# Optimization experiments

Measured on AMD Instinct MI355X. Metric: run time of the kernel, lower is better.

Reference implementation:

```python
import jax, jax.numpy as jnp
import numpy as np

D_MODEL = 512
NUM_HEADS = 8
D_HEAD = 64
B, T = 8, 1024


def sinusoidal_pos(start, end, d, dtype=jnp.float32):
    # positions start .. end-1, standard sinusoidal encoding, shape (1, end-start, d)
    pos = jnp.arange(start, end, dtype=jnp.float32)[:, None]              # (L,1)
    inv_freq = jnp.exp(-jnp.log(10000.0) * jnp.arange(0, d, 2, dtype=jnp.float32) / d)
    ang = pos * inv_freq[None, :]                                          # (L,d/2)
    pe = jnp.stack([jnp.sin(ang), jnp.cos(ang)], axis=-1).reshape(pos.shape[0], d)
    return pe[None].astype(dtype)                                          # (1,L,d)


def _relative_shift(x):
    # x: (B,H,T,L) -> Transformer-XL shift trick
    b, h, t, l = x.shape
    x = jnp.pad(x, ((0, 0), (0, 0), (0, 0), (1, 0)))                       # (B,H,T,L+1)
    x = x.reshape(b, h, l + 1, t)[:, :, 1:, :].reshape(b, h, t, l)
    return x


def setup_inputs() -> dict:
    key = jax.random.key(0)
    ks = jax.random.split(key, 8)
    hd = NUM_HEADS * D_HEAD
    s_in = 1.0 / np.sqrt(D_MODEL)
    s_out = 1.0 / np.sqrt(hd)
    return {
        "xs": jax.random.normal(ks[0], (B, T, D_MODEL), jnp.float32),
        "mask": jnp.ones((B, T, T), jnp.int32),
        "Wq": jax.random.normal(ks[1], (D_MODEL, hd), jnp.float32) * s_in,
        "Wk": jax.random.normal(ks[2], (D_MODEL, hd), jnp.float32) * s_in,
        "Wv": jax.random.normal(ks[3], (D_MODEL, hd), jnp.float32) * s_in,
        "Wpos": jax.random.normal(ks[4], (D_MODEL, hd), jnp.float32) * s_in,
        "Wout": jax.random.normal(ks[5], (hd, D_MODEL), jnp.float32) * s_out,
        "u_bias": jax.random.normal(ks[6], (NUM_HEADS, D_HEAD), jnp.float32) * 0.02,
        "v_bias": jax.random.normal(ks[7], (NUM_HEADS, D_HEAD), jnp.float32) * 0.02,
    }


def reference(xs, mask, Wq, Wk, Wv, Wpos, Wout, u_bias, v_bias):
    b, t, _ = xs.shape
    scale = 1.0 / np.sqrt(D_HEAD)

    def split_heads(y):  # (B,T,H*dh) -> (B,H,T,dh)
        return y.reshape(b, t, NUM_HEADS, D_HEAD).transpose(0, 2, 1, 3)

    q = split_heads(xs @ Wq)
    k = split_heads(xs @ Wk)
    v = split_heads(xs @ Wv)

    # positions -(T-1) .. T-1, length 2T-1
    pos_enc = sinusoidal_pos(-(t - 1), t, D_MODEL, xs.dtype)               # (1,L,D)
    p = (pos_enc[0] @ Wpos).reshape(-1, NUM_HEADS, D_HEAD).transpose(1, 0, 2)  # (H,L,dh)

    q_u = q + u_bias[None, :, None, :]
    q_v = q + v_bias[None, :, None, :]

    matrix_ac = jnp.einsum("bhtd,bhsd->bhts", q_u, k)                      # (B,H,T,T)
    matrix_bd = jnp.einsum("bhtd,hld->bhtl", q_v, p)                       # (B,H,T,2T-1)
    matrix_bd = _relative_shift(matrix_bd)[:, :, :, :t]                    # (B,H,T,T)

    scores = (matrix_ac + matrix_bd) * scale

    m = (mask[:, None, :, :] == 0)                                          # (B,1,T,T)
    scores = jnp.where(m, -jnp.inf, scores)
    attn = jax.nn.softmax(scores, axis=-1)
    attn = jnp.where(m, 0.0, attn)
    # dropout is identity in eval mode

    z = jnp.einsum("bhts,bhsd->bthd", attn, v).reshape(b, t, NUM_HEADS * D_HEAD)
    return z @ Wout
```

## Files before the change

kernel.cpp:

```cpp
#include <hip/hip_runtime.h>
#include <hip/hip_bf16.h>


typedef unsigned short u16;
typedef unsigned long long u64;
typedef unsigned int u32;
typedef __attribute__((ext_vector_type(8))) short bf16x8;
typedef __attribute__((ext_vector_type(8))) unsigned short ushort8v;
typedef __attribute__((ext_vector_type(4))) float floatx4;

__device__ __forceinline__ float b2f(u16 u) {
    union { unsigned int i; float f; } x; x.i = ((unsigned int)u) << 16; return x.f;
}
__device__ __forceinline__ u16 f2b(float f) {
    __hip_bfloat16 h = __float2bfloat16(f);
    return *reinterpret_cast<u16*>(&h);
}

#define MFMA16(a, b, c) __builtin_amdgcn_mfma_f32_16x16x32_bf16(a, b, c, 0, 0, 0)

__device__ __forceinline__ void gll16(const u16* g, u16* l) {
    __builtin_amdgcn_global_load_lds(
        (const __attribute__((address_space(1))) u32*)g,
        (__attribute__((address_space(3))) u32*)l, 16, 0, 0);
}

__global__ __launch_bounds__(256) void prep_kernel(
    const float* __restrict__ X, u16* __restrict__ Xb,
    const float* __restrict__ W0, const float* __restrict__ W1,
    const float* __restrict__ W2, const float* __restrict__ W3,
    const float* __restrict__ W4, u16* __restrict__ WT,
    const int* __restrict__ mask, u64* __restrict__ Mp,
    u16* __restrict__ Peb)
{
    const int bi = blockIdx.x;
    const int tid = threadIdx.x;
    if (bi < 2048) {
        size_t i = ((size_t)bi * 256 + tid) * 8;
        float4 a = *(const float4*)&X[i];
        float4 b = *(const float4*)&X[i + 4];
        ushort8v s;
        s[0] = f2b(a.x); s[1] = f2b(a.y); s[2] = f2b(a.z); s[3] = f2b(a.w);
        s[4] = f2b(b.x); s[5] = f2b(b.y); s[6] = f2b(b.z); s[7] = f2b(b.w);
        *(ushort8v*)&Xb[i] = s;
    } else if (bi < 2368) {
        __shared__ float t[64][68];
        const int li = bi - 2048;
        const int m = li >> 6;
        const float* src = (m == 0) ? W0 : (m == 1) ? W1 : (m == 2) ? W2
                         : (m == 3) ? W3 : W4;
        u16* dst = WT + (size_t)m * 262144;
        const int sub = li & 63;
        const int k0 = ((sub >> 3) & 7) * 64, n0 = (sub & 7) * 64;
        const int r = tid >> 4, c = tid & 15;
#pragma unroll
        for (int rr = 0; rr < 64; rr += 16) {
            float4 v = *(const float4*)&src[(size_t)(k0 + r + rr) * 512 + n0 + 4 * c];
            t[r + rr][4 * c + 0] = v.x;
            t[r + rr][4 * c + 1] = v.y;
            t[r + rr][4 * c + 2] = v.z;
            t[r + rr][4 * c + 3] = v.w;
        }
        __syncthreads();
        const int nrow = tid >> 2, kc = (tid & 3) * 16;
        ushort8v s0, s1;
#pragma unroll
        for (int e = 0; e < 8; ++e) {
            s0[e] = f2b(t[kc + e][nrow]);
            s1[e] = f2b(t[kc + 8 + e][nrow]);
        }
        *(ushort8v*)&dst[(size_t)(n0 + nrow) * 512 + k0 + kc] = s0;
        *(ushort8v*)&dst[(size_t)(n0 + nrow) * 512 + k0 + kc + 8] = s1;
    } else if (bi < 4416) {
        const int lane = tid & 63, w = tid >> 6;
        const int row = (bi - 2368) * 4 + w;
#pragma unroll
        for (int j = 0; j < 16; ++j) {
            int v = mask[(size_t)row * 1024 + j * 64 + lane];
            u64 bits = __ballot(v != 0);
            if (lane == j) Mp[(size_t)row * 16 + j] = bits;
        }
    } else {
        const int lane = tid & 63, w = tid >> 6;
        const int l = (bi - 4416) * 4 + w;
        const int lc = (l > 2046) ? 2046 : l;
        const float pos = (float)(lc - 1023);
        ushort8v s;
#pragma unroll
        for (int e = 0; e < 8; ++e) {
            int k = (lane << 3) + e;
            int i = k >> 1;
            float invf = __expf(-0.035977892f * (float)i);
            float ang = pos * invf;
            float v = (k & 1) ? __cosf(ang) : __sinf(ang);
            s[e] = f2b(v);
        }
        *(ushort8v*)&Peb[(size_t)l * 512 + (lane << 3)] = s;
    }
}

__global__ __launch_bounds__(256, 2) void qkv_mfma(
    const u16* __restrict__ Xb, const u16* __restrict__ WqT,
    const u16* __restrict__ WkT, const u16* __restrict__ WvT,
    const u16* __restrict__ Peb, const u16* __restrict__ WposT,
    u16* __restrict__ Qb, u16* __restrict__ Kb, u16* __restrict__ Vtg,
    u16* __restrict__ Pg)
{
    __shared__ u16 Xl[128 * 40];
    __shared__ u16 Wl[128 * 40];
    const int tid = threadIdx.x;
    const int lane = tid & 63, w = tid >> 6;
    const int quad = lane >> 4, ln = lane & 15;
    const int wm = w & 1, wn = w >> 1;

    const int yy = blockIdx.y;
    int sel, m0, n0;
    const u16 *Ap, *Bp;
    if (yy < 12) {
        sel = yy >> 2; n0 = (yy & 3) * 128; m0 = blockIdx.x * 128;
        Ap = Xb; Bp = (sel == 0) ? WqT : (sel == 1) ? WkT : WvT;
    } else {
        sel = 3; m0 = (blockIdx.x >> 2) * 128; n0 = (blockIdx.x & 3) * 128;
        Ap = Peb; Bp = WposT;
    }
    const int b = (m0 >> 10) & 7, tbase = m0 & 1023;

    const int sr = tid >> 2, sg = tid & 3;

    floatx4 acc[4][4];
#pragma unroll
    for (int i = 0; i < 4; ++i)
#pragma unroll
        for (int j = 0; j < 4; ++j) acc[i][j] = (floatx4){0.f, 0.f, 0.f, 0.f};

    ushort8v xq[2], wq2[2];
#pragma unroll
    for (int it = 0; it < 2; ++it) {
        int r = sr + it * 64;
        xq[it]  = *(const ushort8v*)&Ap[(size_t)(m0 + r) * 512 + sg * 8];
        wq2[it] = *(const ushort8v*)&Bp[(size_t)(n0 + r) * 512 + sg * 8];
    }

    for (int kc = 0; kc < 512; kc += 32) {
        __syncthreads();
#pragma unroll
        for (int it = 0; it < 2; ++it) {
            int r = sr + it * 64;
            *(ushort8v*)&Xl[r * 40 + sg * 8] = xq[it];
            *(ushort8v*)&Wl[r * 40 + sg * 8] = wq2[it];
        }
        __syncthreads();
        if (kc + 32 < 512) {
#pragma unroll
            for (int it = 0; it < 2; ++it) {
                int r = sr + it * 64;
                xq[it]  = *(const ushort8v*)&Ap[(size_t)(m0 + r) * 512 + kc + 32 + sg * 8];
                wq2[it] = *(const ushort8v*)&Bp[(size_t)(n0 + r) * 512 + kc + 32 + sg * 8];
            }
        }
        bf16x8 am[4], an[4];
#pragma unroll
        for (int i = 0; i < 4; ++i)
            am[i] = *(bf16x8*)&Xl[(wm * 64 + i * 16 + ln) * 40 + quad * 8];
#pragma unroll
        for (int j = 0; j < 4; ++j)
            an[j] = *(bf16x8*)&Wl[(wn * 64 + j * 16 + ln) * 40 + quad * 8];
        if (sel != 2) {
#pragma unroll
            for (int i = 0; i < 4; ++i)
#pragma unroll
                for (int j = 0; j < 4; ++j)
                    acc[i][j] = MFMA16(an[j], am[i], acc[i][j]);
        } else {
#pragma unroll
            for (int i = 0; i < 4; ++i)
#pragma unroll
                for (int j = 0; j < 4; ++j)
                    acc[i][j] = MFMA16(am[i], an[j], acc[i][j]);
        }
    }
    if (sel < 2) {
        u16* dst = (sel == 0) ? Qb : Kb;
#pragma unroll
        for (int i = 0; i < 4; ++i) {
            int t = tbase + wm * 64 + i * 16 + ln;
#pragma unroll
            for (int j = 0; j < 4; ++j) {
                int n = n0 + wn * 64 + j * 16 + quad * 4;
                int h = n >> 6, d = n & 63;
                ushort4 s;
                s.x = f2b(acc[i][j][0]); s.y = f2b(acc[i][j][1]);
                s.z = f2b(acc[i][j][2]); s.w = f2b(acc[i][j][3]);
                *(ushort4*)&dst[(((size_t)b * 8 + h) * 1024 + t) * 64 + d] = s;
            }
        }
    } else if (sel == 2) {
#pragma unroll
        for (int i = 0; i < 4; ++i) {
            int t4 = tbase + wm * 64 + i * 16 + quad * 4;
#pragma unroll
            for (int j = 0; j < 4; ++j) {
                int n = n0 + wn * 64 + j * 16 + ln;
                int h = n >> 6, d = n & 63;
                ushort4 s;
                s.x = f2b(acc[i][j][0]); s.y = f2b(acc[i][j][1]);
                s.z = f2b(acc[i][j][2]); s.w = f2b(acc[i][j][3]);
                *(ushort4*)&Vtg[(((size_t)b * 8 + h) * 64 + d) * 1024 + t4] = s;
            }
        }
    } else {
#pragma unroll
        for (int i = 0; i < 4; ++i) {
            int l = m0 + wm * 64 + i * 16 + ln;
#pragma unroll
            for (int j = 0; j < 4; ++j) {
                int n = n0 + wn * 64 + j * 16 + quad * 4;
                int h = n >> 6, d = n & 63;
                ushort4 s;
                s.x = f2b(acc[i][j][0]); s.y = f2b(acc[i][j][1]);
                s.z = f2b(acc[i][j][2]); s.w = f2b(acc[i][j][3]);
                *(ushort4*)&Pg[(((size_t)h << 11) + l) * 64 + d] = s;
            }
        }
    }
}

__device__ __forceinline__ bf16x8 addbias(bf16x8 q, const float* __restrict__ bias) {
    float4 a = *(const float4*)&bias[0];
    float4 b = *(const float4*)&bias[4];
    bf16x8 r;
    r[0] = (short)f2b(0.125f * (b2f((u16)q[0]) + a.x));
    r[1] = (short)f2b(0.125f * (b2f((u16)q[1]) + a.y));
    r[2] = (short)f2b(0.125f * (b2f((u16)q[2]) + a.z));
    r[3] = (short)f2b(0.125f * (b2f((u16)q[3]) + a.w));
    r[4] = (short)f2b(0.125f * (b2f((u16)q[4]) + b.x));
    r[5] = (short)f2b(0.125f * (b2f((u16)q[5]) + b.y));
    r[6] = (short)f2b(0.125f * (b2f((u16)q[6]) + b.z));
    r[7] = (short)f2b(0.125f * (b2f((u16)q[7]) + b.w));
    return r;
}

__global__ __launch_bounds__(256, 2) void attn_mfma(
    const u16* __restrict__ Qb,
    const u16* __restrict__ Kb, const u16* __restrict__ Vtg,
    const u16* __restrict__ P, const u64* __restrict__ Mp,
    const float* __restrict__ ub, const float* __restrict__ vb,
    u16* __restrict__ Z)
{
    __shared__ u16 Klds[64 * 72];
    __shared__ u16 Vtlds[64 * 72];
    __shared__ u16 Pb[256 * 64];
    __shared__ __align__(16) char WaveBuf[4][16 * 84 * 4];

    const int tid  = threadIdx.x;
    const int lane = tid & 63;
    const int w    = tid >> 6;
    const int quad = lane >> 4;
    const int ln   = lane & 15;

    const int bid = blockIdx.x;
    const int xg  = bid & 7;
    const int idx = bid >> 3;
    const int bh_i = xg * 8 + (idx >> 3);
    const int t0 = (idx & 7) << 7;
    const int h  = bh_i & 7;
    const int b  = bh_i >> 3;
    const size_t bh  = (size_t)bh_i * 1024;
    const size_t bhd = (size_t)bh_i * 64;
    const int lbase0 = 896 - t0;
    size_t mprow[2];
    mprow[0] = ((size_t)b * 1024 + t0 + 16 * w + ln) * 16;
    mprow[1] = ((size_t)b * 1024 + t0 + 64 + 16 * w + ln) * 16;

    bf16x8 qu0[2], qu1[2], qv0[2], qv1[2];
#pragma unroll
    for (int c = 0; c < 2; ++c) {
        const size_t qoff = (bh + t0 + 64 * c + 16 * w + ln) * 64;
        bf16x8 q0 = *(const bf16x8*)&Qb[qoff + quad * 8];
        bf16x8 q1 = *(const bf16x8*)&Qb[qoff + 32 + quad * 8];
        qu0[c] = addbias(q0, &ub[h * 64 + quad * 8]);
        qu1[c] = addbias(q1, &ub[h * 64 + 32 + quad * 8]);
        qv0[c] = addbias(q0, &vb[h * 64 + quad * 8]);
        qv1[c] = addbias(q1, &vb[h * 64 + 32 + quad * 8]);
    }

    floatx4 O[2][4];
#pragma unroll
    for (int c = 0; c < 2; ++c)
#pragma unroll
        for (int dt = 0; dt < 4; ++dt) O[c][dt] = (floatx4){0.f, 0.f, 0.f, 0.f};
    float m_run[2] = {-3.0e38f, -3.0e38f}, l_run[2] = {0.f, 0.f};

    float* gw = (float*)&WaveBuf[w][0];
    u16*  pw  = (u16*)&WaveBuf[w][0];

    const int str = tid >> 3, stg = tid & 7;
    const int g8 = lane >> 3, s8 = lane & 7;
    const int pcol = ((s8 ^ g8) << 3);
    ushort8v kq[2], vq[2];
    u64 bc0, bc1;

#pragma unroll
    for (int it = 0; it < 6; ++it) {
        int rb = lbase0 + 8 * w + 32 * it;
        gll16(&P[(((size_t)h << 11) + (size_t)(rb + g8)) * 64 + pcol],
              &Pb[(rb & 255) << 6]);
    }
#pragma unroll
    for (int it = 0; it < 2; ++it) {
        int r = str + it * 32;
        kq[it] = *(const ushort8v*)&Kb[(bh + r) * 64 + stg * 8];
        vq[it] = *(const ushort8v*)&Vtg[(bhd + r) * 1024 + stg * 8];
    }
    bc0 = Mp[mprow[0]];
    bc1 = Mp[mprow[1]];

    for (int s0 = 0; s0 < 1024; s0 += 64) {
        __syncthreads();
#pragma unroll
        for (int it = 0; it < 2; ++it) {
            int r = str + it * 32;
            *(ushort8v*)&Klds[r * 72 + stg * 8] = kq[it];
            *(ushort8v*)&Vtlds[r * 72 + stg * 8] = vq[it];
        }
        __syncthreads();

        const int lb8 = (lbase0 + s0) & 255;
        u64 nb0 = 0, nb1 = 0;
        if (s0 + 64 < 1024) {
#pragma unroll
            for (int it = 0; it < 2; ++it) {
                int r = str + it * 32;
                kq[it] = *(const ushort8v*)&Kb[(bh + s0 + 64 + r) * 64 + stg * 8];
                vq[it] = *(const ushort8v*)&Vtg[(bhd + r) * 1024 + s0 + 64 + stg * 8];
            }
            const int lst = lbase0 + s0 + 192;
#pragma unroll
            for (int it = 0; it < 2; ++it) {
                int rb = lst + 8 * w + 32 * it;
                gll16(&P[(((size_t)h << 11) + (size_t)(rb + g8)) * 64 + pcol],
                      &Pb[(rb & 255) << 6]);
            }
            nb0 = Mp[mprow[0] + (s0 >> 6) + 1];
            nb1 = Mp[mprow[1] + (s0 >> 6) + 1];
        }

        bf16x8 vf0[4], vf1[4];
#pragma unroll
        for (int dt = 0; dt < 4; ++dt) {
            int vr = dt * 16 + ln;
            vf0[dt] = *(bf16x8*)&Vtlds[vr * 72 + quad * 8];
            vf1[dt] = *(bf16x8*)&Vtlds[vr * 72 + 32 + quad * 8];
        }

#pragma unroll
        for (int c = 0; c < 2; ++c) {
            const u64 bits = (c == 0) ? bc0 : bc1;
            const int rb0 = 112 - 64 * c - 16 * w;
            __builtin_amdgcn_s_setprio(1);
#pragma unroll
            for (int jt = 0; jt < 5; ++jt) {
                int rb = rb0 + jt * 16 + ln;
                int prow = ((lb8 + rb) & 255) << 6;
                bf16x8 a0 = *(bf16x8*)&Pb[prow + ((quad ^ (rb & 7)) << 3)];
                bf16x8 a1 = *(bf16x8*)&Pb[prow + (((4 + quad) ^ (rb & 7)) << 3)];
                floatx4 g = {0.f, 0.f, 0.f, 0.f};
                g = MFMA16(a0, qv0[c], g);
                g = MFMA16(a1, qv1[c], g);
                *(floatx4*)&gw[ln * 84 + jt * 16 + quad * 4] = g;
            }
            floatx4 cac[4];
#pragma unroll
            for (int st = 0; st < 4; ++st) {
                int kr = st * 16 + ln;
                bf16x8 a0 = *(bf16x8*)&Klds[kr * 72 + quad * 8];
                bf16x8 a1 = *(bf16x8*)&Klds[kr * 72 + 32 + quad * 8];
                floatx4 cc = {0.f, 0.f, 0.f, 0.f};
                cc = MFMA16(a0, qu0[c], cc);
                cc = MFMA16(a1, qu1[c], cc);
                cac[st] = cc;
            }
            __builtin_amdgcn_s_setprio(0);
            float sc[4][4];
            float cmax = -3.0e38f;
#pragma unroll
            for (int st = 0; st < 4; ++st) {
                int j0 = st * 16 + quad * 4 + 15 - ln;
#pragma unroll
                for (int r = 0; r < 4; ++r) {
                    float v = cac[st][r] + gw[ln * 84 + j0 + r];
                    int ss = st * 16 + quad * 4 + r;
                    v = ((bits >> ss) & 1ull) ? v : -1.0e30f;
                    sc[st][r] = v;
                    cmax = fmaxf(cmax, v);
                }
            }
            cmax = fmaxf(cmax, __shfl_xor(cmax, 16));
            cmax = fmaxf(cmax, __shfl_xor(cmax, 32));
            float m_new = fmaxf(m_run[c], cmax);
            float alpha = __expf(m_run[c] - m_new);
            float psum = 0.f;
#pragma unroll
            for (int st = 0; st < 4; ++st) {
                float p0 = __expf(sc[st][0] - m_new);
                float p1 = __expf(sc[st][1] - m_new);
                float p2 = __expf(sc[st][2] - m_new);
                float p3 = __expf(sc[st][3] - m_new);
                psum += (p0 + p1) + (p2 + p3);
                ushort4 pk;
                pk.x = f2b(p0); pk.y = f2b(p1); pk.z = f2b(p2); pk.w = f2b(p3);
                *(ushort4*)&pw[ln * 72 + st * 16 + quad * 4] = pk;
            }
            psum += __shfl_xor(psum, 16);
            psum += __shfl_xor(psum, 32);
            l_run[c] = l_run[c] * alpha + psum;
            m_run[c] = m_new;
            float a0s = __shfl(alpha, quad * 4 + 0);
            float a1s = __shfl(alpha, quad * 4 + 1);
            float a2s = __shfl(alpha, quad * 4 + 2);
            float a3s = __shfl(alpha, quad * 4 + 3);
#pragma unroll
            for (int dt = 0; dt < 4; ++dt) {
                O[c][dt][0] *= a0s; O[c][dt][1] *= a1s;
                O[c][dt][2] *= a2s; O[c][dt][3] *= a3s;
            }
            bf16x8 pa0 = *(bf16x8*)&pw[ln * 72 + quad * 8];
            bf16x8 pa1 = *(bf16x8*)&pw[ln * 72 + 32 + quad * 8];
            __builtin_amdgcn_s_setprio(1);
#pragma unroll
            for (int dt = 0; dt < 4; ++dt) {
                O[c][dt] = MFMA16(pa0, vf0[dt], O[c][dt]);
                O[c][dt] = MFMA16(pa1, vf1[dt], O[c][dt]);
            }
            __builtin_amdgcn_s_setprio(0);
        }
        bc0 = nb0; bc1 = nb1;
    }
#pragma unroll
    for (int c = 0; c < 2; ++c) {
        float li[4];
#pragma unroll
        for (int r = 0; r < 4; ++r) li[r] = 1.0f / __shfl(l_run[c], quad * 4 + r);
#pragma unroll
        for (int r = 0; r < 4; ++r) {
            size_t zo = ((size_t)b * 1024 + t0 + 64 * c + 16 * w + quad * 4 + r) * 512
                      + h * 64 + ln;
            Z[zo + 0]  = f2b(O[c][0][r] * li[r]);
            Z[zo + 16] = f2b(O[c][1][r] * li[r]);
            Z[zo + 32] = f2b(O[c][2][r] * li[r]);
            Z[zo + 48] = f2b(O[c][3][r] * li[r]);
        }
    }
}

__global__ __launch_bounds__(256, 2) void out_mfma(
    const u16* __restrict__ Zb, const u16* __restrict__ WoT,
    float* __restrict__ out)
{
    __shared__ u16 Xl[128 * 40];
    __shared__ u16 Wl[128 * 40];
    const int tid = threadIdx.x;
    const int lane = tid & 63, w = tid >> 6;
    const int quad = lane >> 4, ln = lane & 15;
    const int wm = w & 1, wn = w >> 1;
    const int m0 = blockIdx.x * 128;
    const int n0 = blockIdx.y * 128;
    const int sr = tid >> 2, sg = tid & 3;

    floatx4 acc[4][4];
#pragma unroll
    for (int i = 0; i < 4; ++i)
#pragma unroll
        for (int j = 0; j < 4; ++j) acc[i][j] = (floatx4){0.f, 0.f, 0.f, 0.f};

    ushort8v xq[2], wq2[2];
#pragma unroll
    for (int it = 0; it < 2; ++it) {
        int r = sr + it * 64;
        xq[it]  = *(const ushort8v*)&Zb[(size_t)(m0 + r) * 512 + sg * 8];
        wq2[it] = *(const ushort8v*)&WoT[(size_t)(n0 + r) * 512 + sg * 8];
    }

    for (int kc = 0; kc < 512; kc += 32) {
        __syncthreads();
#pragma unroll
        for (int it = 0; it < 2; ++it) {
            int r = sr + it * 64;
            *(ushort8v*)&Xl[r * 40 + sg * 8] = xq[it];
            *(ushort8v*)&Wl[r * 40 + sg * 8] = wq2[it];
        }
        __syncthreads();
        if (kc + 32 < 512) {
#pragma unroll
            for (int it = 0; it < 2; ++it) {
                int r = sr + it * 64;
                xq[it]  = *(const ushort8v*)&Zb[(size_t)(m0 + r) * 512 + kc + 32 + sg * 8];
                wq2[it] = *(const ushort8v*)&WoT[(size_t)(n0 + r) * 512 + kc + 32 + sg * 8];
            }
        }
        bf16x8 am[4], an[4];
#pragma unroll
        for (int i = 0; i < 4; ++i)
            am[i] = *(bf16x8*)&Xl[(wm * 64 + i * 16 + ln) * 40 + quad * 8];
#pragma unroll
        for (int j = 0; j < 4; ++j)
            an[j] = *(bf16x8*)&Wl[(wn * 64 + j * 16 + ln) * 40 + quad * 8];
#pragma unroll
        for (int i = 0; i < 4; ++i)
#pragma unroll
            for (int j = 0; j < 4; ++j)
                acc[i][j] = MFMA16(an[j], am[i], acc[i][j]);
    }
#pragma unroll
    for (int i = 0; i < 4; ++i) {
        int m = m0 + wm * 64 + i * 16 + ln;
#pragma unroll
        for (int j = 0; j < 4; ++j) {
            int n = n0 + wn * 64 + j * 16 + quad * 4;
            float4 s;
            s.x = acc[i][j][0]; s.y = acc[i][j][1];
            s.z = acc[i][j][2]; s.w = acc[i][j][3];
            *(float4*)&out[(size_t)m * 512 + n] = s;
        }
    }
}

extern "C" void kernel_launch(void* const* d_in, const int* in_sizes, int n_in,
                              void* d_out, int out_size, void* d_ws, size_t ws_size,
                              hipStream_t stream) {
    const float* xs   = (const float*)d_in[0];
    const int*   mask = (const int*)d_in[1];
    const float* Wq   = (const float*)d_in[2];
    const float* Wk   = (const float*)d_in[3];
    const float* Wv   = (const float*)d_in[4];
    const float* Wpos = (const float*)d_in[5];
    const float* Wout = (const float*)d_in[6];
    const float* ub   = (const float*)d_in[7];
    const float* vb   = (const float*)d_in[8];
    float* out = (float*)d_out;

    u16* Qb  = (u16*)d_ws;
    u16* Kb  = Qb + 4194304;
    u16* Vtg = Kb + 4194304;
    u16* Pg  = Vtg + 4194304;
    u16* XZ  = Pg + 1048576;
    u16* WT  = XZ + 4194304;
    u16* WqT = WT;
    u16* WkT = WT + 262144;
    u16* WvT = WT + 524288;
    u16* WoT = WT + 786432;
    u16* WposT = WT + 1048576;
    u16* Peb = WT + 1310720;
    u64* Mp  = (u64*)(Peb + 1048576);

    prep_kernel<<<4928, 256, 0, stream>>>(xs, XZ, Wq, Wk, Wv, Wout, Wpos, WT,
                                          mask, Mp, Peb);
    qkv_mfma<<<dim3(64, 13), 256, 0, stream>>>(XZ, WqT, WkT, WvT, Peb, WposT,
                                               Qb, Kb, Vtg, Pg);
    attn_mfma<<<512, 256, 0, stream>>>(Qb, Kb, Vtg, Pg, Mp, ub, vb, XZ);
    out_mfma<<<dim3(64, 4), 256, 0, stream>>>(XZ, WoT, out);
}
```

Baseline: 217.3 us.

## Load QKV GEMM tiles directly into LDS with XOR swizzle

```diff
diff --git a/kernel.cpp b/kernel.cpp
--- a/kernel.cpp
+++ b/kernel.cpp
@@ -99,15 +99,15 @@
     }
 }
 
-__global__ __launch_bounds__(256, 2) void qkv_mfma(
+__global__ __launch_bounds__(256, 3) void qkv_mfma(
     const u16* __restrict__ Xb, const u16* __restrict__ WqT,
     const u16* __restrict__ WkT, const u16* __restrict__ WvT,
     const u16* __restrict__ Peb, const u16* __restrict__ WposT,
     u16* __restrict__ Qb, u16* __restrict__ Kb, u16* __restrict__ Vtg,
     u16* __restrict__ Pg)
 {
-    __shared__ u16 Xl[128 * 40];
-    __shared__ u16 Wl[128 * 40];
+    __shared__ u16 Xl[128 * 32];
+    __shared__ u16 Wl[128 * 32];
     const int tid = threadIdx.x;
     const int lane = tid & 63, w = tid >> 6;
     const int quad = lane >> 4, ln = lane & 15;
@@ -125,7 +125,7 @@
     }
     const int b = (m0 >> 10) & 7, tbase = m0 & 1023;
 
-    const int sr = tid >> 2, sg = tid & 3;
+    const int sdr = lane >> 2, sds = lane & 3;
 
     floatx4 acc[4][4];
 #pragma unroll
@@ -133,38 +133,29 @@
 #pragma unroll
         for (int j = 0; j < 4; ++j) acc[i][j] = (floatx4){0.f, 0.f, 0.f, 0.f};
 
-    ushort8v xq[2], wq2[2];
-#pragma unroll
-    for (int it = 0; it < 2; ++it) {
-        int r = sr + it * 64;
-        xq[it]  = *(const ushort8v*)&Ap[(size_t)(m0 + r) * 512 + sg * 8];
-        wq2[it] = *(const ushort8v*)&Bp[(size_t)(n0 + r) * 512 + sg * 8];
-    }
-
     for (int kc = 0; kc < 512; kc += 32) {
         __syncthreads();
 #pragma unroll
-        for (int it = 0; it < 2; ++it) {
-            int r = sr + it * 64;
-            *(ushort8v*)&Xl[r * 40 + sg * 8] = xq[it];
-            *(ushort8v*)&Wl[r * 40 + sg * 8] = wq2[it];
-        }
-        __syncthreads();
-        if (kc + 32 < 512) {
-#pragma unroll
-            for (int it = 0; it < 2; ++it) {
-                int r = sr + it * 64;
-                xq[it]  = *(const ushort8v*)&Ap[(size_t)(m0 + r) * 512 + kc + 32 + sg * 8];
-                wq2[it] = *(const ushort8v*)&Bp[(size_t)(n0 + r) * 512 + kc + 32 + sg * 8];
-            }
-        }
+        for (int c2 = 0; c2 < 2; ++c2) {
+            const int r0 = w * 32 + c2 * 16;
+            const int r  = r0 + sdr;
+            const int scol = ((sds ^ ((r >> 1) & 3)) << 3);
+            gll16(&Ap[(size_t)(m0 + r) * 512 + kc + scol], &Xl[r0 * 32]);
+            gll16(&Bp[(size_t)(n0 + r) * 512 + kc + scol], &Wl[r0 * 32]);
+        }
+        __syncthreads();
+
         bf16x8 am[4], an[4];
 #pragma unroll
-        for (int i = 0; i < 4; ++i)
-            am[i] = *(bf16x8*)&Xl[(wm * 64 + i * 16 + ln) * 40 + quad * 8];
-#pragma unroll
-        for (int j = 0; j < 4; ++j)
-            an[j] = *(bf16x8*)&Wl[(wn * 64 + j * 16 + ln) * 40 + quad * 8];
+        for (int i = 0; i < 4; ++i) {
+            int rr = wm * 64 + i * 16 + ln;
+            am[i] = *(bf16x8*)&Xl[rr * 32 + ((quad ^ ((rr >> 1) & 3)) << 3)];
+        }
+#pragma unroll
+        for (int j = 0; j < 4; ++j) {
+            int rr = wn * 64 + j * 16 + ln;
+            an[j] = *(bf16x8*)&Wl[rr * 32 + ((quad ^ ((rr >> 1) & 3)) << 3)];
+        }
         if (sel != 2) {
 #pragma unroll
             for (int i = 0; i < 4; ++i)
```

New measurement: 238.4 us. 9.7% more time.

## Double-buffer K via async global-to-LDS loads and read V directly from global

Applied to the files above, without the earlier changes.

```diff
diff --git a/kernel.cpp b/kernel.cpp
--- a/kernel.cpp
+++ b/kernel.cpp
@@ -247,8 +247,7 @@
     const float* __restrict__ ub, const float* __restrict__ vb,
     u16* __restrict__ Z)
 {
-    __shared__ u16 Klds[64 * 72];
-    __shared__ u16 Vtlds[64 * 72];
+    __shared__ u16 Klds[2][64 * 64];
     __shared__ u16 Pb[256 * 64];
     __shared__ __align__(16) char WaveBuf[4][16 * 84 * 4];
 
@@ -294,10 +293,8 @@
     float* gw = (float*)&WaveBuf[w][0];
     u16*  pw  = (u16*)&WaveBuf[w][0];
 
-    const int str = tid >> 3, stg = tid & 7;
     const int g8 = lane >> 3, s8 = lane & 7;
     const int pcol = ((s8 ^ g8) << 3);
-    ushort8v kq[2], vq[2];
     u64 bc0, bc1;
 
 #pragma unroll
@@ -308,31 +305,33 @@
     }
 #pragma unroll
     for (int it = 0; it < 2; ++it) {
-        int r = str + it * 32;
-        kq[it] = *(const ushort8v*)&Kb[(bh + r) * 64 + stg * 8];
-        vq[it] = *(const ushort8v*)&Vtg[(bhd + r) * 1024 + stg * 8];
+        int r0 = w * 16 + it * 8;
+        gll16(&Kb[(bh + r0 + g8) * 64 + pcol], &Klds[0][r0 * 64]);
     }
     bc0 = Mp[mprow[0]];
     bc1 = Mp[mprow[1]];
 
-    for (int s0 = 0; s0 < 1024; s0 += 64) {
+    for (int i = 0; i < 16; ++i) {
+        const int s0 = i << 6;
         __syncthreads();
-#pragma unroll
-        for (int it = 0; it < 2; ++it) {
-            int r = str + it * 32;
-            *(ushort8v*)&Klds[r * 72 + stg * 8] = kq[it];
-            *(ushort8v*)&Vtlds[r * 72 + stg * 8] = vq[it];
-        }
-        __syncthreads();
-
+        const u16* kl = &Klds[i & 1][0];
         const int lb8 = (lbase0 + s0) & 255;
+
+        bf16x8 vf0[4], vf1[4];
+#pragma unroll
+        for (int dt = 0; dt < 4; ++dt) {
+            const u16* vp = &Vtg[(bhd + dt * 16 + ln) * 1024 + s0 + quad * 8];
+            vf0[dt] = *(const bf16x8*)(vp);
+            vf1[dt] = *(const bf16x8*)(vp + 32);
+        }
+
         u64 nb0 = 0, nb1 = 0;
-        if (s0 + 64 < 1024) {
+        if (i < 15) {
 #pragma unroll
             for (int it = 0; it < 2; ++it) {
-                int r = str + it * 32;
-                kq[it] = *(const ushort8v*)&Kb[(bh + s0 + 64 + r) * 64 + stg * 8];
-                vq[it] = *(const ushort8v*)&Vtg[(bhd + r) * 1024 + s0 + 64 + stg * 8];
+                int r0 = w * 16 + it * 8;
+                gll16(&Kb[(bh + s0 + 64 + r0 + g8) * 64 + pcol],
+                      &Klds[(i + 1) & 1][r0 * 64]);
             }
             const int lst = lbase0 + s0 + 192;
 #pragma unroll
@@ -341,16 +340,8 @@
                 gll16(&P[(((size_t)h << 11) + (size_t)(rb + g8)) * 64 + pcol],
                       &Pb[(rb & 255) << 6]);
             }
-            nb0 = Mp[mprow[0] + (s0 >> 6) + 1];
-            nb1 = Mp[mprow[1] + (s0 >> 6) + 1];
-        }
-
-        bf16x8 vf0[4], vf1[4];
-#pragma unroll
-        for (int dt = 0; dt < 4; ++dt) {
-            int vr = dt * 16 + ln;
-            vf0[dt] = *(bf16x8*)&Vtlds[vr * 72 + quad * 8];
-            vf1[dt] = *(bf16x8*)&Vtlds[vr * 72 + 32 + quad * 8];
+            nb0 = Mp[mprow[0] + i + 1];
+            nb1 = Mp[mprow[1] + i + 1];
         }
 
 #pragma unroll
@@ -373,8 +364,8 @@
 #pragma unroll
             for (int st = 0; st < 4; ++st) {
                 int kr = st * 16 + ln;
-                bf16x8 a0 = *(bf16x8*)&Klds[kr * 72 + quad * 8];
-                bf16x8 a1 = *(bf16x8*)&Klds[kr * 72 + 32 + quad * 8];
+                bf16x8 a0 = *(bf16x8*)&kl[kr * 64 + ((quad ^ (kr & 7)) << 3)];
+                bf16x8 a1 = *(bf16x8*)&kl[kr * 64 + (((4 + quad) ^ (kr & 7)) << 3)];
                 floatx4 cc = {0.f, 0.f, 0.f, 0.f};
                 cc = MFMA16(a0, qu0[c], cc);
                 cc = MFMA16(a1, qu1[c], cc);
```

After: 219.4 us. No clear change (+0.9%).
